# Performance work log

Hardware: AMD Instinct MI355X
Metric: run time of the kernel (lower is better)

## Reference

```python
import jax, jax.numpy as jnp
import numpy as np

IMAGE_C = 1
IMAGE_W = 28
PIXELS_PER_ROW = IMAGE_W * IMAGE_C  # 28

B, T, E = 16, IMAGE_W * IMAGE_W * IMAGE_C, 512  # T = 784
H = 8
D = E // H  # head_dim = 64


def get_2d_causal_bias(T):
    idx = jnp.arange(T)
    i = idx // PIXELS_PER_ROW          # row index
    j = (idx % PIXELS_PER_ROW) // IMAGE_C  # col index
    c = idx % IMAGE_C                  # channel index
    q_i, k_i = i[:, None], i[None, :]
    q_j, k_j = j[:, None], j[None, :]
    q_c, k_c = c[:, None], c[None, :]
    allowed = (k_i < q_i) | ((k_i == q_i) & (k_j < q_j)) | (
        (k_i == q_i) & (k_j == q_j) & (k_c <= q_c))
    bias = jnp.where(allowed, 0.0, -jnp.inf).astype(jnp.float32)
    return bias[None, None]  # [1, 1, T, T]


def setup_inputs() -> dict:
    key = jax.random.key(0)
    ks = jax.random.split(key, 5)
    s = 1.0 / np.sqrt(E)
    return {
        "x": jax.random.normal(ks[0], (B, T, E), dtype=jnp.float32),
        "Wq": jax.random.normal(ks[1], (E, E), dtype=jnp.float32) * s,
        "bq": jnp.zeros((E,), dtype=jnp.float32),
        "Wk": jax.random.normal(ks[2], (E, E), dtype=jnp.float32) * s,
        "bk": jnp.zeros((E,), dtype=jnp.float32),
        "Wv": jax.random.normal(ks[3], (E, E), dtype=jnp.float32) * s,
        "bv": jnp.zeros((E,), dtype=jnp.float32),
        "Wo": jax.random.normal(ks[4], (E, E), dtype=jnp.float32) * s,
        "bo": jnp.zeros((E,), dtype=jnp.float32),
    }


def reference(x, Wq, bq, Wk, bk, Wv, bv, Wo, bo):
    Bx, Tx, Ex = x.shape
    # projections (torch Linear: y = x @ W.T + b; here W stored as [E, E] used directly)
    Q = (x @ Wq + bq).reshape(Bx, Tx, H, D).transpose(0, 2, 1, 3)  # [B,H,T,D]
    K = (x @ Wk + bk).reshape(Bx, Tx, H, D).transpose(0, 2, 1, 3)
    V = (x @ Wv + bv).reshape(Bx, Tx, H, D).transpose(0, 2, 1, 3)
    scores = jnp.einsum("bhqd,bhkd->bhqk", Q, K) / jnp.sqrt(jnp.float32(D))
    scores = scores + get_2d_causal_bias(Tx)
    attn = jax.nn.softmax(scores, axis=-1)
    ctx = jnp.einsum("bhqk,bhkd->bhqd", attn, V)
    ctx = ctx.transpose(0, 2, 1, 3).reshape(Bx, Tx, Ex)
    return ctx @ Wo + bo
```

## Files before the change

kernel.cpp:

```cpp
#include <hip/hip_runtime.h>
#include <hip/hip_bf16.h>

#define BB    16
#define TT    784
#define TPK   832
#define TPQ   896
#define EE    512
#define HH    8
#define DD    64
#define BT    (BB*TT)

typedef short short8 __attribute__((ext_vector_type(8)));
typedef short short4v __attribute__((ext_vector_type(4)));
typedef float floatx4 __attribute__((ext_vector_type(4)));
typedef float floatx16 __attribute__((ext_vector_type(16)));
typedef unsigned uint4v __attribute__((ext_vector_type(4)));

__device__ __forceinline__ short f2bf(float f) {
    unsigned u = __builtin_bit_cast(unsigned, f);
    u += 0x7FFFu + ((u >> 16) & 1u);
    return (short)(u >> 16);
}

__device__ __forceinline__ unsigned cvtpk_bf16(float lo, float hi) {
    unsigned r;
    asm("v_cvt_pk_bf16_f32 %0, %1, %2" : "=v"(r) : "v"(lo), "v"(hi));
    return r;
}

__device__ __forceinline__ void gload_lds16(const short* g, short* l) {
    __builtin_amdgcn_global_load_lds(
        (const __attribute__((address_space(1))) void*)g,
        (__attribute__((address_space(3))) void*)l, 16, 0, 0);
}

__global__ void prep_kernel(const float* __restrict__ x, short* __restrict__ xb,
                            const float* __restrict__ Wq, const float* __restrict__ Wk,
                            const float* __restrict__ Wv, short* __restrict__ wqkvt,
                            const float* __restrict__ Wo, short* __restrict__ wot,
                            short* __restrict__ Qb, short* __restrict__ Kb, short* __restrict__ Vt)
{
    __shared__ short t[64][65];
    int b = blockIdx.x;
    if (b < 3136) {
        int i = (b * 256 + threadIdx.x) * 8;
        float4 a = *(const float4*)(x + i);
        float4 c = *(const float4*)(x + i + 4);
        short8 o;
        o[0] = f2bf(a.x); o[1] = f2bf(a.y); o[2] = f2bf(a.z); o[3] = f2bf(a.w);
        o[4] = f2bf(c.x); o[5] = f2bf(c.y); o[6] = f2bf(c.z); o[7] = f2bf(c.w);
        *(short8*)(xb + i) = o;
    } else if (b < 3392) {
        const float* W; short* out; int n0, k0;
        if (b < 3328) {
            int tt = b - 3136;
            n0 = (tt % 24) * 64; k0 = (tt / 24) * 64;
            W = (n0 < 512) ? Wq : (n0 < 1024 ? Wk : Wv);
            out = wqkvt;
        } else {
            int tt = b - 3328;
            n0 = (tt % 8) * 64; k0 = (tt / 8) * 64;
            W = Wo; out = wot;
        }
        int nn0 = n0 & 511;
        for (int i = threadIdx.x; i < 4096; i += 256) {
            int r = i >> 6, c = i & 63;
            t[r][c] = f2bf(W[(k0 + r) * 512 + nn0 + c]);
        }
        __syncthreads();
        for (int i = threadIdx.x; i < 4096; i += 256) {
            int nr = i >> 6, kc = i & 63;
            out[(n0 + nr) * 512 + k0 + kc] = t[kc][nr];
        }
    } else {
        int c = (b - 3392) * 256 + threadIdx.x;
        short8 z = (short8){0,0,0,0,0,0,0,0};
        if (c < 114688) {
            int bh = c / 896, j = c - bh * 896;
            *(short8*)&Qb[(bh * TPQ + TT) * 64 + j * 8] = z;
        } else if (c < 163840) {
            int c2 = c - 114688;
            int bh = c2 / 384, j = c2 - bh * 384;
            *(short8*)&Kb[(bh * TPK + TT) * 64 + j * 8] = z;
        } else {
            int c3 = c - 163840;
            int bh = c3 / 384, j = c3 - bh * 384;
            int d = j / 6, m = j - d * 6;
            *(short8*)&Vt[(bh * 64 + d) * TPK + TT + m * 8] = z;
        }
    }
}

__global__ __launch_bounds__(256, 4) void gemm_qkv_kernel(
    const short* __restrict__ A, const short* __restrict__ Bt,
    const float* __restrict__ bq, const float* __restrict__ bk, const float* __restrict__ bv,
    short* __restrict__ Qb, short* __restrict__ Kb, short* __restrict__ Vt)
{
    __shared__ __align__(16) short smem[16640];
    short* As0 = smem;
    short* Bs0 = smem + 8192;

    const int m0 = blockIdx.x * 128, n0 = blockIdx.y * 128;
    const int tid = threadIdx.x;
    const int lane = tid & 63, w = tid >> 6;
    const int wr = w >> 1, wc = w & 1;
    const int l16 = lane & 15, quad = lane >> 4;

    const int srow = w * 32 + (lane >> 2);
    const int scol = (lane & 3) * 8;
    const short* Ag = A  + (size_t)(m0 + srow) * 512 + scol;
    const short* Bg = Bt + (size_t)(n0 + srow) * 512 + scol;
    short* Abase = As0 + w * 1024;
    short* Bbase = Bs0 + w * 1024;

    auto stage = [&](int it) {
        int b = it & 1;
        int ko = it * 32;
        gload_lds16(Ag + ko,            Abase + b * 4096);
        gload_lds16(Ag + ko + 16 * 512, Abase + b * 4096 + 512);
        gload_lds16(Bg + ko,            Bbase + b * 4096);
        gload_lds16(Bg + ko + 16 * 512, Bbase + b * 4096 + 512);
    };

    floatx4 acc[4][4];
    #pragma unroll
    for (int i = 0; i < 4; i++)
        #pragma unroll
        for (int j = 0; j < 4; j++)
            acc[i][j] = (floatx4){0.f, 0.f, 0.f, 0.f};

    stage(0);
    __syncthreads();

    for (int it = 0; it < 16; it++) {
        if (it < 15) stage(it + 1);
        const short* as = As0 + (it & 1) * 4096;
        const short* bs = Bs0 + (it & 1) * 4096;
        short8 af[4], bf[4];
        #pragma unroll
        for (int i = 0; i < 4; i++) {
            af[i] = *(const short8*)&as[(wr * 64 + i * 16 + l16) * 32 + quad * 8];
            bf[i] = *(const short8*)&bs[(wc * 64 + i * 16 + l16) * 32 + quad * 8];
        }
        #pragma unroll
        for (int mi = 0; mi < 4; mi++)
            #pragma unroll
            for (int ni = 0; ni < 4; ni++)
                acc[mi][ni] = __builtin_amdgcn_mfma_f32_16x16x32_bf16(af[mi], bf[ni], acc[mi][ni], 0, 0, 0);
        __syncthreads();
    }

    const int sel = n0 >> 9;
    if (sel == 2) {
        #pragma unroll
        for (int mi = 0; mi < 4; mi++) {
            int m = m0 + wr * 64 + mi * 16 + quad * 4;
            int bb = m / TT, t = m - bb * TT;
            #pragma unroll
            for (int ni = 0; ni < 4; ni++) {
                int nn = (n0 + wc * 64 + ni * 16 + l16) & 511;
                int hh = nn >> 6, dd = nn & 63;
                float b = bv[nn];
                short4v pv;
                #pragma unroll
                for (int r = 0; r < 4; r++) pv[r] = f2bf(acc[mi][ni][r] + b);
                *(short4v*)&Vt[((size_t)(bb * HH + hh) * 64 + dd) * TPK + t] = pv;
            }
        }
    } else {
        short* Ct = smem;
        const float* bias = (sel == 0) ? bq : bk;
        #pragma unroll
        for (int mi = 0; mi < 4; mi++) {
            #pragma unroll
            for (int ni = 0; ni < 4; ni++) {
                int nl = wc * 64 + ni * 16 + l16;
                int nn = (n0 + nl) & 511;
                float b = bias[nn];
                #pragma unroll
                for (int r = 0; r < 4; r++) {
                    float v = acc[mi][ni][r] + b;
                    if (sel == 0) v *= 0.125f;
                    Ct[(wr * 64 + mi * 16 + quad * 4 + r) * 130 + nl] = f2bf(v);
                }
            }
        }
        __syncthreads();
        short* dst = (sel == 0) ? Qb : Kb;
        const int tp = (sel == 0) ? TPQ : TPK;
        int nl = lane * 2;
        int nn = (n0 + nl) & 511;
        int hh = nn >> 6, dd = nn & 63;
        #pragma unroll 4
        for (int rr = 0; rr < 32; rr++) {
            int ml = w * 32 + rr;
            int m = m0 + ml;
            int bb = m / TT, t = m - bb * TT;
            unsigned pv = *(const unsigned*)&Ct[ml * 130 + nl];
            *(unsigned*)&dst[((bb * HH + hh) * tp + t) * 64 + dd] = pv;
        }
    }
}

__global__ __launch_bounds__(256, 3) void attn_kernel(
    const short* __restrict__ Qb, const short* __restrict__ Kb, const short* __restrict__ Vt,
    short* __restrict__ ctx)
{
    const int g = blockIdx.x;
    const int low = g & 7, rest = g >> 3;
    const int qt = 12 - (rest >> 4);
    const int bh = ((rest & 15) << 3) | low;
    const int bb = bh >> 3, hh = bh & 7;
    const int tid = threadIdx.x;
    const int lane = tid & 63, w = tid >> 6;
    const int wq = w >> 1, wk = w & 1;
    const int l32 = lane & 31, hi = lane >> 5;
    const int r7 = l32 & 7;

    __shared__ __align__(16) short Ks[2][4096];
    __shared__ __align__(16) short Vs[2][4096];

    const short* Kbase = Kb + (size_t)(bh * TPK) * 64;
    const short* Vbase = Vt + (size_t)(bh * 64) * TPK;

    const int srow = tid >> 3;
    const int sc8  = tid & 7;
    const int scol = sc8 * 8;
    const int ksw  = (sc8 ^ (srow & 7)) * 8;
    const int vg0  = (sc8 >> 1) * 2;
    const int vsw0 = ((vg0       ^ (srow & 7)) * 8) + (sc8 & 1) * 4;
    const int vsw1 = (((vg0 + 1) ^ (srow & 7)) * 8) + (sc8 & 1) * 4;

    short8 kreg[2], vreg[2];
    auto load_tile = [&](int kt) {
        #pragma unroll
        for (int p = 0; p < 2; p++) {
            int row = srow + p * 32;
            kreg[p] = *(const short8*)(Kbase + (kt * 64 + row) * 64 + scol);
            vreg[p] = *(const short8*)(Vbase + row * TPK + kt * 64 + scol);
        }
    };
    auto store_tile = [&](int b) {
        #pragma unroll
        for (int p = 0; p < 2; p++) {
            int ro = (srow + p * 32) * 64;
            *(short8*)&Ks[b][ro + ksw] = kreg[p];
            short4v v0, v1;
            #pragma unroll
            for (int i = 0; i < 4; i++) { v0[i] = vreg[p][i]; v1[i] = vreg[p][i + 4]; }
            *(short4v*)&Vs[b][ro + vsw0] = v0;
            *(short4v*)&Vs[b][ro + vsw1] = v1;
        }
    };

    const int q_lo = qt * 64 + wq * 32;
    const int qg = q_lo + l32;
    const bool wreal = (q_lo < TT);
    const short* Qrow = Qb + (size_t)(bh * TPQ + qg) * 64;
    short8 qf[4];
    #pragma unroll
    for (int d = 0; d < 4; d++) qf[d] = *(const short8*)(Qrow + d * 16 + hi * 8);

    floatx16 accO[2];
    #pragma unroll
    for (int dt = 0; dt < 2; dt++)
        #pragma unroll
        for (int i = 0; i < 16; i++) accO[dt][i] = 0.f;
    float accL = 0.f;

    load_tile(0);
    store_tile(0);

    for (int kt = 0; kt <= qt; kt++) {
        const int cb = kt & 1;
        if (kt < qt) load_tile(kt + 1);
        __syncthreads();
        const int kbase = kt * 64 + wk * 32;
        if (wreal && kbase <= q_lo + 31) {
            floatx16 z;
            #pragma unroll
            for (int i = 0; i < 16; i++) z[i] = 0.f;
            #pragma unroll
            for (int d = 0; d < 4; d++) {
                short8 kf = *(const short8*)&Ks[cb][(wk * 32 + l32) * 64 + (((d * 2 + hi) ^ r7) * 8)];
                z = __builtin_amdgcn_mfma_f32_32x32x16_bf16(kf, qf[d], z, 0, 0, 0);
            }
            float p[16];
            #pragma unroll
            for (int r = 0; r < 16; r++) p[r] = __expf(z[r]);
            if (kbase + 31 > q_lo) {
                #pragma unroll
                for (int r = 0; r < 16; r++) {
                    int keyg = kbase + (r & 3) + 8 * (r >> 2) + 4 * hi;
                    if (keyg > qg) p[r] = 0.f;
                }
            }
            #pragma unroll
            for (int r = 0; r < 16; r++) accL += p[r];
            #pragma unroll
            for (int s = 0; s < 2; s++) {
                uint4v pw;
                #pragma unroll
                for (int jj = 0; jj < 4; jj++)
                    pw[jj] = cvtpk_bf16(p[8 * s + 2 * jj], p[8 * s + 2 * jj + 1]);
                short8 pb = __builtin_bit_cast(short8, pw);
                #pragma unroll
                for (int dt = 0; dt < 2; dt++) {
                    short8 vf = *(const short8*)&Vs[cb][(dt * 32 + l32) * 64 + (((wk * 4 + s * 2 + hi) ^ r7) * 8)];
                    accO[dt] = __builtin_amdgcn_mfma_f32_32x32x16_bf16(vf, pb, accO[dt], 0, 0, 0);
                }
            }
        }
        if (kt < qt) store_tile((kt + 1) & 1);
    }

    __syncthreads();
    float* rbuf  = (float*)&Ks[0][0];
    float* rbufL = (float*)&Vs[0][0];
    if (wk == 1) {
        #pragma unroll
        for (int dt = 0; dt < 2; dt++)
            #pragma unroll
            for (int r = 0; r < 16; r++)
                rbuf[((wq * 2 + dt) * 16 + r) * 64 + lane] = accO[dt][r];
        rbufL[wq * 64 + lane] = accL;
    }
    __syncthreads();
    if (wk == 0) {
        #pragma unroll
        for (int dt = 0; dt < 2; dt++)
            #pragma unroll
            for (int r = 0; r < 16; r++)
                accO[dt][r] += rbuf[((wq * 2 + dt) * 16 + r) * 64 + lane];
        accL += rbufL[wq * 64 + lane];
        float Lt = accL + __shfl_xor(accL, 32, 64);
        if (wreal && qg < TT) {
            float inv = 1.f / Lt;
            short* crow = ctx + (size_t)(bb * TT + qg) * 512 + hh * 64;
            #pragma unroll
            for (int dt = 0; dt < 2; dt++)
                #pragma unroll
                for (int g4 = 0; g4 < 4; g4++) {
                    short4v pv;
                    #pragma unroll
                    for (int r4 = 0; r4 < 4; r4++) pv[r4] = f2bf(accO[dt][g4 * 4 + r4] * inv);
                    *(short4v*)&crow[dt * 32 + g4 * 8 + 4 * hi] = pv;
                }
        }
    }
}

__global__ __launch_bounds__(256, 4) void gemm_out_kernel(
    const short* __restrict__ A, const short* __restrict__ Bt,
    const float* __restrict__ bo, float* __restrict__ out)
{
    __shared__ __align__(16) short smem[16384];
    short* As0 = smem;
    short* Bs0 = smem + 8192;

    const int m0 = blockIdx.x * 128, n0 = blockIdx.y * 128;
    const int tid = threadIdx.x;
    const int lane = tid & 63, w = tid >> 6;
    const int wr = w >> 1, wc = w & 1;
    const int l16 = lane & 15, quad = lane >> 4;

    const int srow = w * 32 + (lane >> 2);
    const int scol = (lane & 3) * 8;
    const short* Ag = A  + (size_t)(m0 + srow) * 512 + scol;
    const short* Bg = Bt + (size_t)(n0 + srow) * 512 + scol;
    short* Abase = As0 + w * 1024;
    short* Bbase = Bs0 + w * 1024;

    auto stage = [&](int it) {
        int b = it & 1;
        int ko = it * 32;
        gload_lds16(Ag + ko,            Abase + b * 4096);
        gload_lds16(Ag + ko + 16 * 512, Abase + b * 4096 + 512);
        gload_lds16(Bg + ko,            Bbase + b * 4096);
        gload_lds16(Bg + ko + 16 * 512, Bbase + b * 4096 + 512);
    };

    floatx4 acc[4][4];
    #pragma unroll
    for (int i = 0; i < 4; i++)
        #pragma unroll
        for (int j = 0; j < 4; j++)
            acc[i][j] = (floatx4){0.f, 0.f, 0.f, 0.f};

    stage(0);
    __syncthreads();

    for (int it = 0; it < 16; it++) {
        if (it < 15) stage(it + 1);
        const short* as = As0 + (it & 1) * 4096;
        const short* bs = Bs0 + (it & 1) * 4096;
        short8 af[4], bf[4];
        #pragma unroll
        for (int i = 0; i < 4; i++) {
            af[i] = *(const short8*)&as[(wr * 64 + i * 16 + l16) * 32 + quad * 8];
            bf[i] = *(const short8*)&bs[(wc * 64 + i * 16 + l16) * 32 + quad * 8];
        }
        #pragma unroll
        for (int mi = 0; mi < 4; mi++)
            #pragma unroll
            for (int ni = 0; ni < 4; ni++)
                acc[mi][ni] = __builtin_amdgcn_mfma_f32_16x16x32_bf16(af[mi], bf[ni], acc[mi][ni], 0, 0, 0);
        __syncthreads();
    }

    #pragma unroll
    for (int mi = 0; mi < 4; mi++) {
        #pragma unroll
        for (int ni = 0; ni < 4; ni++) {
            int n = n0 + wc * 64 + ni * 16 + l16;
            float bias = bo[n];
            #pragma unroll
            for (int r = 0; r < 4; r++) {
                int m = m0 + wr * 64 + mi * 16 + quad * 4 + r;
                out[(size_t)m * 512 + n] = acc[mi][ni][r] + bias;
            }
        }
    }
}

extern "C" void kernel_launch(void* const* d_in, const int* in_sizes, int n_in,
                              void* d_out, int out_size, void* d_ws, size_t ws_size,
                              hipStream_t stream) {
    const float* x  = (const float*)d_in[0];
    const float* Wq = (const float*)d_in[1];
    const float* bq = (const float*)d_in[2];
    const float* Wk = (const float*)d_in[3];
    const float* bk = (const float*)d_in[4];
    const float* Wv = (const float*)d_in[5];
    const float* bv = (const float*)d_in[6];
    const float* Wo = (const float*)d_in[7];
    const float* bo = (const float*)d_in[8];
    float* out = (float*)d_out;

    char* ws = (char*)d_ws;
    size_t off = 0;
    auto alloc = [&](size_t bytes) -> void* {
        void* p = ws + off;
        off += (bytes + 255) & ~(size_t)255;
        return p;
    };
    short* xb    = (short*)alloc((size_t)BT * EE * 2);
    short* wqkvt = (short*)alloc((size_t)1536 * 512 * 2);
    short* wot   = (short*)alloc((size_t)512 * 512 * 2);
    short* Qb    = (short*)alloc((size_t)BB * HH * TPQ * DD * 2);
    short* Kb    = (short*)alloc((size_t)BB * HH * TPK * DD * 2);
    short* Vtb   = (short*)alloc((size_t)BB * HH * DD * TPK * 2);
    short* ctxb  = (short*)alloc((size_t)BT * EE * 2);

    prep_kernel<<<4224, 256, 0, stream>>>(x, xb, Wq, Wk, Wv, wqkvt, Wo, wot, Qb, Kb, Vtb);
    gemm_qkv_kernel<<<dim3(98, 12), 256, 0, stream>>>(xb, wqkvt, bq, bk, bv, Qb, Kb, Vtb);
    attn_kernel<<<1664, 256, 0, stream>>>(Qb, Kb, Vtb, ctxb);
    gemm_out_kernel<<<dim3(98, 4), 256, 0, stream>>>(ctxb, wot, bo, out);
}
```

Baseline: 162.6 us.

## Fuse all four stages into one persistent cooperative kernel with grid syncs

Replaces the four separate launches (prep, QKV GEMM, attention, output GEMM) with a single persistent cooperative kernel that separates the stages with grid-wide barriers. The QKV GEMM and attention stages pull work items from atomic counters so blocks balance dynamically. This is meant to remove launch gaps and per-kernel tail effects, at the cost of grid.sync overhead, capped occupancy (launch_bounds 256,3 and at most 1024 blocks) and register pressure from merging all stage code into one kernel. If the cooperative launch fails, it falls back to the old four-kernel path.

```diff
diff --git a/kernel.cpp b/kernel.cpp
--- a/kernel.cpp
+++ b/kernel.cpp
@@ -1,5 +1,8 @@
 #include <hip/hip_runtime.h>
 #include <hip/hip_bf16.h>
+#include <hip/hip_cooperative_groups.h>
+
+namespace cg = cooperative_groups;
 
 #define BB    16
 #define TT    784
@@ -32,6 +35,410 @@
     __builtin_amdgcn_global_load_lds(
         (const __attribute__((address_space(1))) void*)g,
         (__attribute__((address_space(3))) void*)l, 16, 0, 0);
+}
+
+__global__ __launch_bounds__(256, 3) void fused_kernel(
+    const float* __restrict__ x,  short* __restrict__ xb,
+    const float* __restrict__ Wq, const float* __restrict__ Wk,
+    const float* __restrict__ Wv, short* __restrict__ wqkvt,
+    const float* __restrict__ Wo, short* __restrict__ wot,
+    const float* __restrict__ bq, const float* __restrict__ bk,
+    const float* __restrict__ bv,
+    short* __restrict__ Qb, short* __restrict__ Kb, short* __restrict__ Vt,
+    short* __restrict__ ctx, const float* __restrict__ bo,
+    float* __restrict__ out, int* __restrict__ ctrs)
+{
+    cg::grid_group gg = cg::this_grid();
+    __shared__ __align__(16) short smem[16640];
+    __shared__ int s_u;
+
+    const int tid  = threadIdx.x;
+    const int lane = tid & 63, w = tid >> 6;
+    const int l16  = lane & 15, quad = lane >> 4;
+
+    if (blockIdx.x == 0 && tid == 0) { ctrs[0] = 0; ctrs[1] = 0; }
+    for (int u = blockIdx.x; u < 4224; u += gridDim.x) {
+        if (u < 3136) {
+            int i = (u * 256 + tid) * 8;
+            float4 a = *(const float4*)(x + i);
+            float4 c = *(const float4*)(x + i + 4);
+            short8 o;
+            o[0] = f2bf(a.x); o[1] = f2bf(a.y); o[2] = f2bf(a.z); o[3] = f2bf(a.w);
+            o[4] = f2bf(c.x); o[5] = f2bf(c.y); o[6] = f2bf(c.z); o[7] = f2bf(c.w);
+            *(short8*)(xb + i) = o;
+        } else if (u < 3392) {
+            short (*t)[65] = (short(*)[65])smem;
+            const float* W; short* outp; int n0, k0;
+            if (u < 3328) {
+                int tt = u - 3136;
+                n0 = (tt % 24) * 64; k0 = (tt / 24) * 64;
+                W = (n0 < 512) ? Wq : (n0 < 1024 ? Wk : Wv);
+                outp = wqkvt;
+            } else {
+                int tt = u - 3328;
+                n0 = (tt % 8) * 64; k0 = (tt / 8) * 64;
+                W = Wo; outp = wot;
+            }
+            int nn0 = n0 & 511;
+            __syncthreads();
+            for (int i = tid; i < 4096; i += 256) {
+                int r = i >> 6, c = i & 63;
+                t[r][c] = f2bf(W[(k0 + r) * 512 + nn0 + c]);
+            }
+            __syncthreads();
+            for (int i = tid; i < 4096; i += 256) {
+                int nr = i >> 6, kc = i & 63;
+                outp[(n0 + nr) * 512 + k0 + kc] = t[kc][nr];
+            }
+            __syncthreads();
+        } else {
+            int c = (u - 3392) * 256 + tid;
+            short8 z = (short8){0,0,0,0,0,0,0,0};
+            if (c < 114688) {
+                int bh = c / 896, j = c - bh * 896;
+                *(short8*)&Qb[(bh * TPQ + TT) * 64 + j * 8] = z;
+            } else if (c < 163840) {
+                int c2 = c - 114688;
+                int bh = c2 / 384, j = c2 - bh * 384;
+                *(short8*)&Kb[(bh * TPK + TT) * 64 + j * 8] = z;
+            } else {
+                int c3 = c - 163840;
+                int bh = c3 / 384, j = c3 - bh * 384;
+                int d = j / 6, m = j - d * 6;
+                *(short8*)&Vt[(bh * 64 + d) * TPK + TT + m * 8] = z;
+            }
+        }
+    }
+    __threadfence();
+    gg.sync();
+
+    {
+        short* As0 = smem;
+        short* Bs0 = smem + 8192;
+        const int wr = w >> 1, wc = w & 1;
+        const int srow = w * 32 + (lane >> 2);
+        const int scol = (lane & 3) * 8;
+        short* Abase = As0 + w * 1024;
+        short* Bbase = Bs0 + w * 1024;
+
+        for (;;) {
+            if (tid == 0) s_u = atomicAdd(&ctrs[0], 1);
+            __syncthreads();
+            int u = s_u;
+            __syncthreads();
+            if (u >= 1176) break;
+            const int m0 = (u % 98) * 128, n0 = (u / 98) * 128;
+
+            const short* Ag = xb    + (size_t)(m0 + srow) * 512 + scol;
+            const short* Bg = wqkvt + (size_t)(n0 + srow) * 512 + scol;
+            auto stage = [&](int it) {
+                int b = it & 1;
+                int ko = it * 32;
+                gload_lds16(Ag + ko,            Abase + b * 4096);
+                gload_lds16(Ag + ko + 16 * 512, Abase + b * 4096 + 512);
+                gload_lds16(Bg + ko,            Bbase + b * 4096);
+                gload_lds16(Bg + ko + 16 * 512, Bbase + b * 4096 + 512);
+            };
+
+            floatx4 acc[4][4];
+            #pragma unroll
+            for (int i = 0; i < 4; i++)
+                #pragma unroll
+                for (int j = 0; j < 4; j++)
+                    acc[i][j] = (floatx4){0.f, 0.f, 0.f, 0.f};
+
+            stage(0);
+            __syncthreads();
+            for (int it = 0; it < 16; it++) {
+                if (it < 15) stage(it + 1);
+                const short* as = As0 + (it & 1) * 4096;
+                const short* bs = Bs0 + (it & 1) * 4096;
+                short8 af[4], bf[4];
+                #pragma unroll
+                for (int i = 0; i < 4; i++) {
+                    af[i] = *(const short8*)&as[(wr * 64 + i * 16 + l16) * 32 + quad * 8];
+                    bf[i] = *(const short8*)&bs[(wc * 64 + i * 16 + l16) * 32 + quad * 8];
+                }
+                #pragma unroll
+                for (int mi = 0; mi < 4; mi++)
+                    #pragma unroll
+                    for (int ni = 0; ni < 4; ni++)
+                        acc[mi][ni] = __builtin_amdgcn_mfma_f32_16x16x32_bf16(af[mi], bf[ni], acc[mi][ni], 0, 0, 0);
+                __syncthreads();
+            }
+
+            const int sel = n0 >> 9;
+            if (sel == 2) {
+                #pragma unroll
+                for (int mi = 0; mi < 4; mi++) {
+                    int m = m0 + wr * 64 + mi * 16 + quad * 4;
+                    int bb = m / TT, t = m - bb * TT;
+                    #pragma unroll
+                    for (int ni = 0; ni < 4; ni++) {
+                        int nn = (n0 + wc * 64 + ni * 16 + l16) & 511;
+                        int hh = nn >> 6, dd = nn & 63;
+                        float b = bv[nn];
+                        short4v pv;
+                        #pragma unroll
+                        for (int r = 0; r < 4; r++) pv[r] = f2bf(acc[mi][ni][r] + b);
+                        *(short4v*)&Vt[((size_t)(bb * HH + hh) * 64 + dd) * TPK + t] = pv;
+                    }
+                }
+            } else {
+                short* Ct = smem;
+                const float* bias = (sel == 0) ? bq : bk;
+                #pragma unroll
+                for (int mi = 0; mi < 4; mi++) {
+                    #pragma unroll
+                    for (int ni = 0; ni < 4; ni++) {
+                        int nl = wc * 64 + ni * 16 + l16;
+                        int nn = (n0 + nl) & 511;
+                        float b = bias[nn];
+                        #pragma unroll
+                        for (int r = 0; r < 4; r++) {
+                            float v = acc[mi][ni][r] + b;
+                            if (sel == 0) v *= 0.125f;
+                            Ct[(wr * 64 + mi * 16 + quad * 4 + r) * 130 + nl] = f2bf(v);
+                        }
+                    }
+                }
+                __syncthreads();
+                short* dst = (sel == 0) ? Qb : Kb;
+                const int tp = (sel == 0) ? TPQ : TPK;
+                int nl = lane * 2;
+                int nn = (n0 + nl) & 511;
+                int hh = nn >> 6, dd = nn & 63;
+                #pragma unroll 4
+                for (int rr = 0; rr < 32; rr++) {
+                    int ml = w * 32 + rr;
+                    int m = m0 + ml;
+                    int bb = m / TT, t = m - bb * TT;
+                    unsigned pv = *(const unsigned*)&Ct[ml * 130 + nl];
+                    *(unsigned*)&dst[((bb * HH + hh) * tp + t) * 64 + dd] = pv;
+                }
+            }
+            __syncthreads();
+        }
+    }
+    __threadfence();
+    gg.sync();
+
+    {
+        short* KsA = smem;
+        short* VsA = smem + 8192;
+        const int wq = w >> 1, wk = w & 1;
+        const int l32 = lane & 31, hi = lane >> 5;
+        const int r7 = l32 & 7;
+
+        const int srow = tid >> 3;
+        const int sc8  = tid & 7;
+        const int scol = sc8 * 8;
+        const int ksw  = (sc8 ^ (srow & 7)) * 8;
+        const int vg0  = (sc8 >> 1) * 2;
+        const int vsw0 = ((vg0       ^ (srow & 7)) * 8) + (sc8 & 1) * 4;
+        const int vsw1 = (((vg0 + 1) ^ (srow & 7)) * 8) + (sc8 & 1) * 4;
+
+        for (;;) {
+            if (tid == 0) s_u = atomicAdd(&ctrs[1], 1);
+            __syncthreads();
+            int u = s_u;
+            __syncthreads();
+            if (u >= 1664) break;
+            const int qt = 12 - (u >> 7);
+            const int bh = u & 127;
+            const int bb = bh >> 3, hh = bh & 7;
+
+            const short* Kbase = Kb + (size_t)(bh * TPK) * 64;
+            const short* Vbase = Vt + (size_t)(bh * 64) * TPK;
+
+            short8 kreg[2], vreg[2];
+            auto load_tile = [&](int kt) {
+                #pragma unroll
+                for (int p = 0; p < 2; p++) {
+                    int row = srow + p * 32;
+                    kreg[p] = *(const short8*)(Kbase + (kt * 64 + row) * 64 + scol);
+                    vreg[p] = *(const short8*)(Vbase + row * TPK + kt * 64 + scol);
+                }
+            };
+            auto store_tile = [&](int b) {
+                #pragma unroll
+                for (int p = 0; p < 2; p++) {
+                    int ro = (srow + p * 32) * 64;
+                    *(short8*)&KsA[b * 4096 + ro + ksw] = kreg[p];
+                    short4v v0, v1;
+                    #pragma unroll
+                    for (int i = 0; i < 4; i++) { v0[i] = vreg[p][i]; v1[i] = vreg[p][i + 4]; }
+                    *(short4v*)&VsA[b * 4096 + ro + vsw0] = v0;
+                    *(short4v*)&VsA[b * 4096 + ro + vsw1] = v1;
+                }
+            };
+
+            const int q_lo = qt * 64 + wq * 32;
+            const int qg = q_lo + l32;
+            const bool wreal = (q_lo < TT);
+            const short* Qrow = Qb + (size_t)(bh * TPQ + qg) * 64;
+            short8 qf[4];
+            #pragma unroll
+            for (int d = 0; d < 4; d++) qf[d] = *(const short8*)(Qrow + d * 16 + hi * 8);
+
+            floatx16 accO[2];
+            #pragma unroll
+            for (int dt = 0; dt < 2; dt++)
+                #pragma unroll
+                for (int i = 0; i < 16; i++) accO[dt][i] = 0.f;
+            float accL = 0.f;
+
+            load_tile(0);
+            store_tile(0);
+
+            for (int kt = 0; kt <= qt; kt++) {
+                const int cb = kt & 1;
+                if (kt < qt) load_tile(kt + 1);
+                __syncthreads();
+                const int kbase = kt * 64 + wk * 32;
+                if (wreal && kbase <= q_lo + 31) {
+                    floatx16 z;
+                    #pragma unroll
+                    for (int i = 0; i < 16; i++) z[i] = 0.f;
+                    #pragma unroll
+                    for (int d = 0; d < 4; d++) {
+                        short8 kf = *(const short8*)&KsA[cb * 4096 + (wk * 32 + l32) * 64 + (((d * 2 + hi) ^ r7) * 8)];
+                        z = __builtin_amdgcn_mfma_f32_32x32x16_bf16(kf, qf[d], z, 0, 0, 0);
+                    }
+                    float p[16];
+                    #pragma unroll
+                    for (int r = 0; r < 16; r++) p[r] = __expf(z[r]);
+                    if (kbase + 31 > q_lo) {
+                        #pragma unroll
+                        for (int r = 0; r < 16; r++) {
+                            int keyg = kbase + (r & 3) + 8 * (r >> 2) + 4 * hi;
+                            if (keyg > qg) p[r] = 0.f;
+                        }
+                    }
+                    #pragma unroll
+                    for (int r = 0; r < 16; r++) accL += p[r];
+                    #pragma unroll
+                    for (int s = 0; s < 2; s++) {
+                        uint4v pw;
+                        #pragma unroll
+                        for (int jj = 0; jj < 4; jj++)
+                            pw[jj] = cvtpk_bf16(p[8 * s + 2 * jj], p[8 * s + 2 * jj + 1]);
+                        short8 pb = __builtin_bit_cast(short8, pw);
+                        #pragma unroll
+                        for (int dt = 0; dt < 2; dt++) {
+                            short8 vf = *(const short8*)&VsA[cb * 4096 + (dt * 32 + l32) * 64 + (((wk * 4 + s * 2 + hi) ^ r7) * 8)];
+                            accO[dt] = __builtin_amdgcn_mfma_f32_32x32x16_bf16(vf, pb, accO[dt], 0, 0, 0);
+                        }
+                    }
+                }
+                if (kt < qt) store_tile((kt + 1) & 1);
+            }
+
+            __syncthreads();
+            float* rbuf  = (float*)KsA;
+            float* rbufL = (float*)VsA;
+            if (wk == 1) {
+                #pragma unroll
+                for (int dt = 0; dt < 2; dt++)
+                    #pragma unroll
+                    for (int r = 0; r < 16; r++)
+                        rbuf[((wq * 2 + dt) * 16 + r) * 64 + lane] = accO[dt][r];
+                rbufL[wq * 64 + lane] = accL;
+            }
+            __syncthreads();
+            if (wk == 0) {
+                #pragma unroll
+                for (int dt = 0; dt < 2; dt++)
+                    #pragma unroll
+                    for (int r = 0; r < 16; r++)
+                        accO[dt][r] += rbuf[((wq * 2 + dt) * 16 + r) * 64 + lane];
+                accL += rbufL[wq * 64 + lane];
+                float Lt = accL + __shfl_xor(accL, 32, 64);
+                if (wreal && qg < TT) {
+                    float inv = 1.f / Lt;
+                    short* crow = ctx + (size_t)(bb * TT + qg) * 512 + hh * 64;
+                    #pragma unroll
+                    for (int dt = 0; dt < 2; dt++)
+                        #pragma unroll
+                        for (int g4 = 0; g4 < 4; g4++) {
+                            short4v pv;
+                            #pragma unroll
+                            for (int r4 = 0; r4 < 4; r4++) pv[r4] = f2bf(accO[dt][g4 * 4 + r4] * inv);
+                            *(short4v*)&crow[dt * 32 + g4 * 8 + 4 * hi] = pv;
+                        }
+                }
+            }
+            __syncthreads();
+        }
+    }
+    __threadfence();
+    gg.sync();
+
+    {
+        short* As0 = smem;
+        short* Bs0 = smem + 8192;
+        const int wr = w >> 1, wc = w & 1;
+        const int srow = w * 32 + (lane >> 2);
+        const int scol = (lane & 3) * 8;
+        short* Abase = As0 + w * 1024;
+        short* Bbase = Bs0 + w * 1024;
+
+        for (int u3 = blockIdx.x; u3 < 392; u3 += gridDim.x) {
+            const int m0 = (u3 % 98) * 128, n0 = (u3 / 98) * 128;
+            const short* Ag = ctx + (size_t)(m0 + srow) * 512 + scol;
+            const short* Bg = wot + (size_t)(n0 + srow) * 512 + scol;
+
+            auto stage = [&](int it) {
+                int b = it & 1;
+                int ko = it * 32;
+                gload_lds16(Ag + ko,            Abase + b * 4096);
+                gload_lds16(Ag + ko + 16 * 512, Abase + b * 4096 + 512);
+                gload_lds16(Bg + ko,            Bbase + b * 4096);
+                gload_lds16(Bg + ko + 16 * 512, Bbase + b * 4096 + 512);
+            };
+
+            floatx4 acc[4][4];
+            #pragma unroll
+            for (int i = 0; i < 4; i++)
+                #pragma unroll
+                for (int j = 0; j < 4; j++)
+                    acc[i][j] = (floatx4){0.f, 0.f, 0.f, 0.f};
+
+            stage(0);
+            __syncthreads();
+            for (int it = 0; it < 16; it++) {
+                if (it < 15) stage(it + 1);
+                const short* as = As0 + (it & 1) * 4096;
+                const short* bs = Bs0 + (it & 1) * 4096;
+                short8 af[4], bf[4];
+                #pragma unroll
+                for (int i = 0; i < 4; i++) {
+                    af[i] = *(const short8*)&as[(wr * 64 + i * 16 + l16) * 32 + quad * 8];
+                    bf[i] = *(const short8*)&bs[(wc * 64 + i * 16 + l16) * 32 + quad * 8];
+                }
+                #pragma unroll
+                for (int mi = 0; mi < 4; mi++)
+                    #pragma unroll
+                    for (int ni = 0; ni < 4; ni++)
+                        acc[mi][ni] = __builtin_amdgcn_mfma_f32_16x16x32_bf16(af[mi], bf[ni], acc[mi][ni], 0, 0, 0);
+                __syncthreads();
+            }
+
+            #pragma unroll
+            for (int mi = 0; mi < 4; mi++) {
+                #pragma unroll
+                for (int ni = 0; ni < 4; ni++) {
+                    int n = n0 + wc * 64 + ni * 16 + l16;
+                    float bias = bo[n];
+                    #pragma unroll
+                    for (int r = 0; r < 4; r++) {
+                        int m = m0 + wr * 64 + mi * 16 + quad * 4 + r;
+                        out[(size_t)m * 512 + n] = acc[mi][ni][r] + bias;
+                    }
+                }
+            }
+        }
+    }
 }
 
 __global__ void prep_kernel(const float* __restrict__ x, short* __restrict__ xb,
@@ -451,9 +858,48 @@
     short* Kb    = (short*)alloc((size_t)BB * HH * TPK * DD * 2);
     short* Vtb   = (short*)alloc((size_t)BB * HH * DD * TPK * 2);
     short* ctxb  = (short*)alloc((size_t)BT * EE * 2);
-
-    prep_kernel<<<4224, 256, 0, stream>>>(x, xb, Wq, Wk, Wv, wqkvt, Wo, wot, Qb, Kb, Vtb);
-    gemm_qkv_kernel<<<dim3(98, 12), 256, 0, stream>>>(xb, wqkvt, bq, bk, bv, Qb, Kb, Vtb);
-    attn_kernel<<<1664, 256, 0, stream>>>(Qb, Kb, Vtb, ctxb);
-    gemm_out_kernel<<<dim3(98, 4), 256, 0, stream>>>(ctxb, wot, bo, out);
+    int*   ctrs  = (int*)alloc(256);
+
+    static int coop_grid = -1;
+    if (coop_grid < 0) {
+        int dev = 0;
+        (void)hipGetDevice(&dev);
+        int numCU = 0;
+        (void)hipDeviceGetAttribute(&numCU, hipDeviceAttributeMultiprocessorCount, dev);
+        int perCU = 0;
+        hipError_t e = hipOccupancyMaxActiveBlocksPerMultiprocessor(
+            &perCU, (const void*)fused_kernel, 256, 0);
+        if (e == hipSuccess && perCU > 0 && numCU > 0) {
+            long cap = (long)perCU * (long)numCU;
+            coop_grid = (int)(cap < 1024 ? cap : 1024);
+        } else {
+            coop_grid = 0;
+            (void)hipGetLastError();
+        }
+    }
+
+    bool done = false;
+    if (coop_grid > 0) {
+        void* args[] = {
+            (void*)&x, (void*)&xb, (void*)&Wq, (void*)&Wk, (void*)&Wv, (void*)&wqkvt,
+            (void*)&Wo, (void*)&wot, (void*)&bq, (void*)&bk, (void*)&bv,
+            (void*)&Qb, (void*)&Kb, (void*)&Vtb, (void*)&ctxb, (void*)&bo,
+            (void*)&out, (void*)&ctrs
+        };
+        hipError_t err = hipLaunchCooperativeKernel((const void*)fused_kernel,
+                                                    dim3(coop_grid), dim3(256), args, 0, stream);
+        if (err == hipSuccess) {
+            done = true;
+        } else {
+            (void)hipGetLastError();
+            coop_grid = 0;
+        }
+    }
+
+    if (!done) {
+        prep_kernel<<<4224, 256, 0, stream>>>(x, xb, Wq, Wk, Wv, wqkvt, Wo, wot, Qb, Kb, Vtb);
+        gemm_qkv_kernel<<<dim3(98, 12), 256, 0, stream>>>(xb, wqkvt, bq, bk, bv, Qb, Kb, Vtb);
+        attn_kernel<<<1664, 256, 0, stream>>>(Qb, Kb, Vtb, ctxb);
+        gemm_out_kernel<<<dim3(98, 4), 256, 0, stream>>>(ctxb, wot, bo, out);
+    }
 }
```

Result: slower. 414.8 us (+155.2%).
